# Kernel optimization log

Hardware: AMD Instinct MI355X
Metric: run time of the kernel (lower is better)

The kernel has to match this reference:

```python
import jax, jax.numpy as jnp
import numpy as np

N = 50000   # nodes
E = 640000  # edges
IN_C, HID_C, OUT_C = 128, 128, 64


def _glorot(key, shape):
    lim = float(np.sqrt(6.0 / (shape[0] + shape[1])))
    return jax.random.uniform(key, shape, jnp.float32, -lim, lim)


def setup_inputs() -> dict:
    key = jax.random.key(0)
    ks = jax.random.split(key, 6)
    x = jax.random.normal(ks[0], (N, IN_C), jnp.float32)
    edge_index = jax.random.randint(ks[1], (2, E), 0, N, dtype=jnp.int64)
    W1 = _glorot(ks[2], (IN_C, HID_C));  b1 = jnp.zeros((HID_C,), jnp.float32)
    W2 = _glorot(ks[3], (HID_C, HID_C)); b2 = jnp.zeros((HID_C,), jnp.float32)
    W3 = _glorot(ks[4], (HID_C, OUT_C)); b3 = jnp.zeros((OUT_C,), jnp.float32)
    return {"x": x, "edge_index": edge_index,
            "W1": W1, "b1": b1, "W2": W2, "b2": b2, "W3": W3, "b3": b3}


def gcn_conv(x, W, b, src, dst, n_nodes):
    """PyG GCNConv (eval): add self-loops, D^-1/2 (A+I) D^-1/2, linear, bias."""
    h = x @ W  # [N, out]
    ones = jnp.ones(src.shape[0], h.dtype)
    # degree including the self-loop (+1 per node)
    deg = jax.ops.segment_sum(ones, dst, num_segments=n_nodes) + 1.0
    dinv_sqrt = jax.lax.rsqrt(deg)
    coef = dinv_sqrt[src] * dinv_sqrt[dst]               # [E]
    agg = jax.ops.segment_sum(h[src] * coef[:, None], dst, num_segments=n_nodes)
    agg = agg + h * (1.0 / deg)[:, None]                 # self-loop term: 1/deg[i]
    return agg + b


def reference(x, edge_index, W1, b1, W2, b2, W3, b3):
    src, dst = edge_index[0], edge_index[1]
    h = jax.nn.relu(gcn_conv(x, W1, b1, src, dst, N))
    h = jax.nn.relu(gcn_conv(h, W2, b2, src, dst, N))
    return gcn_conv(h, W3, b3, src, dst, N)
```

## Files before the change

kernel.cpp:

```cpp
#include <hip/hip_runtime.h>


#define K_DIM 128

__device__ __forceinline__ unsigned short f2bf(float x) {
    unsigned u = __float_as_uint(x);
    return (unsigned short)((u + 0x7fffu + ((u >> 16) & 1u)) >> 16);
}
__device__ __forceinline__ float bflo(unsigned v) { return __uint_as_float(v << 16); }
__device__ __forceinline__ float bfhi(unsigned v) { return __uint_as_float(v & 0xffff0000u); }


__global__ void k_zero_int(int* __restrict__ p, int n) {
    int i = blockIdx.x * 256 + threadIdx.x;
    if (i < n) p[i] = 0;
}

__global__ void k_count(const int* __restrict__ dst, int* __restrict__ cnt, int E) {
    int e = blockIdx.x * 256 + threadIdx.x;
    if (e < E) atomicAdd(&cnt[dst[e]], 1);
}

__global__ void k_norms(const int* __restrict__ cnt, float* __restrict__ rsd, int n) {
    int i = blockIdx.x * 256 + threadIdx.x;
    if (i < n) rsd[i] = rsqrtf((float)cnt[i] + 1.0f);
}

__global__ void k_scan_block(const int* __restrict__ cnt, int* __restrict__ rowptr,
                             int* __restrict__ bsum, int n) {
    __shared__ int s[256];
    int t = threadIdx.x;
    int i = blockIdx.x * 256 + t;
    int x = (i < n) ? cnt[i] : 0;
    s[t] = x;
    __syncthreads();
#pragma unroll
    for (int d = 1; d < 256; d <<= 1) {
        int v = (t >= d) ? s[t - d] : 0;
        __syncthreads();
        s[t] += v;
        __syncthreads();
    }
    if (i < n) rowptr[i] = s[t] - x;
    if (t == 255) bsum[blockIdx.x] = s[255];
}

__global__ void k_scan_bsums(int* __restrict__ bsum, int nb) {
    __shared__ int s[256];
    int t = threadIdx.x;
    int x = (t < nb) ? bsum[t] : 0;
    s[t] = x;
    __syncthreads();
#pragma unroll
    for (int d = 1; d < 256; d <<= 1) {
        int v = (t >= d) ? s[t - d] : 0;
        __syncthreads();
        s[t] += v;
        __syncthreads();
    }
    if (t < nb) bsum[t] = s[t] - x;
}

__global__ void k_scan_add(int* __restrict__ rowptr, int* __restrict__ cursor,
                           const int* __restrict__ bsum, int n, int E) {
    int i = blockIdx.x * 256 + threadIdx.x;
    if (i < n) {
        int v = rowptr[i] + bsum[i >> 8];
        rowptr[i] = v;
        cursor[i] = v;
    }
    if (i == 0) rowptr[n] = E;
}

__global__ void k_fill(const int* __restrict__ src, const int* __restrict__ dst,
                       int* __restrict__ cursor, int* __restrict__ col, int E) {
    int e = blockIdx.x * 256 + threadIdx.x;
    if (e < E) {
        int d = dst[e];
        int pos = atomicAdd(&cursor[d], 1);
        col[pos] = src[e];
    }
}

template <int COUT>
__launch_bounds__(256)
__global__ void k_gemm1(const float* __restrict__ X, const float* __restrict__ W,
                        const float* __restrict__ rsd,
                        unsigned short* __restrict__ Hb, int nrows) {
    constexpr int BM = 64, BK = 32, TN = 4;
    constexpr int CG = COUT / TN;
    constexpr int RG = 256 / CG;
    constexpr int TM = BM / RG;
    constexpr int BMP = 68;

    __shared__ float Xs[BK][BMP];
    __shared__ float Ws[BK][COUT];

    const int tid = threadIdx.x;
    const int tx = tid % CG;
    const int ty = tid / CG;
    const int r0 = blockIdx.x * BM;

    float acc[TM][TN];
#pragma unroll
    for (int i = 0; i < TM; ++i)
#pragma unroll
        for (int j = 0; j < TN; ++j) acc[i][j] = 0.0f;

    for (int kb = 0; kb < K_DIM; kb += BK) {
        __syncthreads();
        {
            int r = tid >> 3, kq = tid & 7;
#pragma unroll
            for (int p = 0; p < 2; ++p) {
                int rr = r + p * 32;
                int grow = r0 + rr;
                if (grow >= nrows) grow = nrows - 1;
                float4 v = *(const float4*)&X[(size_t)grow * K_DIM + kb + kq * 4];
                Xs[kq * 4 + 0][rr] = v.x;
                Xs[kq * 4 + 1][rr] = v.y;
                Xs[kq * 4 + 2][rr] = v.z;
                Xs[kq * 4 + 3][rr] = v.w;
            }
        }
        {
            constexpr int F4 = COUT / 4;
            constexpr int RP = 256 / F4;
            int wq = tid % F4, wr = tid / F4;
#pragma unroll
            for (int p = 0; p < BK / RP; ++p) {
                int krow = wr + p * RP;
                *(float4*)&Ws[krow][wq * 4] =
                    *(const float4*)&W[(size_t)(kb + krow) * COUT + wq * 4];
            }
        }
        __syncthreads();
#pragma unroll
        for (int kk = 0; kk < BK; ++kk) {
            float4 w4 = *(const float4*)&Ws[kk][tx * TN];
            float a[TM];
#pragma unroll
            for (int i = 0; i < TM; i += 4) {
                float4 a4 = *(const float4*)&Xs[kk][ty * TM + i];
                a[i] = a4.x; a[i + 1] = a4.y; a[i + 2] = a4.z; a[i + 3] = a4.w;
            }
#pragma unroll
            for (int i = 0; i < TM; ++i) {
                acc[i][0] += a[i] * w4.x;
                acc[i][1] += a[i] * w4.y;
                acc[i][2] += a[i] * w4.z;
                acc[i][3] += a[i] * w4.w;
            }
        }
    }

#pragma unroll
    for (int i = 0; i < TM; ++i) {
        int row = r0 + ty * TM + i;
        if (row < nrows) {
            float rs = rsd[row];
            ushort4 hb;
            hb.x = f2bf(acc[i][0] * rs);
            hb.y = f2bf(acc[i][1] * rs);
            hb.z = f2bf(acc[i][2] * rs);
            hb.w = f2bf(acc[i][3] * rs);
            *(ushort4*)&Hb[(size_t)row * COUT + tx * TN] = hb;
        }
    }
}

template <int COUT>
__launch_bounds__(256)
__global__ void k_gemm_bf(const unsigned short* __restrict__ Ab, const float* __restrict__ W,
                          const float* __restrict__ rsd,
                          unsigned short* __restrict__ Hb, int nrows) {
    constexpr int BM = 64, BK = 32, TN = 4;
    constexpr int CG = COUT / TN;
    constexpr int RG = 256 / CG;
    constexpr int TM = BM / RG;
    constexpr int BMP = 68;

    __shared__ float Xs[BK][BMP];
    __shared__ float Ws[BK][COUT];

    const int tid = threadIdx.x;
    const int tx = tid % CG;
    const int ty = tid / CG;
    const int r0 = blockIdx.x * BM;

    float acc[TM][TN];
#pragma unroll
    for (int i = 0; i < TM; ++i)
#pragma unroll
        for (int j = 0; j < TN; ++j) acc[i][j] = 0.0f;

    for (int kb = 0; kb < K_DIM; kb += BK) {
        __syncthreads();
        {
            int r = tid >> 2, kq = tid & 3;
            int grow = r0 + r;
            if (grow >= nrows) grow = nrows - 1;
            uint4 v = *(const uint4*)&Ab[(size_t)grow * K_DIM + kb + kq * 8];
            int k0 = kq * 8;
            Xs[k0 + 0][r] = bflo(v.x); Xs[k0 + 1][r] = bfhi(v.x);
            Xs[k0 + 2][r] = bflo(v.y); Xs[k0 + 3][r] = bfhi(v.y);
            Xs[k0 + 4][r] = bflo(v.z); Xs[k0 + 5][r] = bfhi(v.z);
            Xs[k0 + 6][r] = bflo(v.w); Xs[k0 + 7][r] = bfhi(v.w);
        }
        {
            constexpr int F4 = COUT / 4;
            constexpr int RP = 256 / F4;
            int wq = tid % F4, wr = tid / F4;
#pragma unroll
            for (int p = 0; p < BK / RP; ++p) {
                int krow = wr + p * RP;
                *(float4*)&Ws[krow][wq * 4] =
                    *(const float4*)&W[(size_t)(kb + krow) * COUT + wq * 4];
            }
        }
        __syncthreads();
#pragma unroll
        for (int kk = 0; kk < BK; ++kk) {
            float4 w4 = *(const float4*)&Ws[kk][tx * TN];
            float a[TM];
#pragma unroll
            for (int i = 0; i < TM; i += 4) {
                float4 a4 = *(const float4*)&Xs[kk][ty * TM + i];
                a[i] = a4.x; a[i + 1] = a4.y; a[i + 2] = a4.z; a[i + 3] = a4.w;
            }
#pragma unroll
            for (int i = 0; i < TM; ++i) {
                acc[i][0] += a[i] * w4.x;
                acc[i][1] += a[i] * w4.y;
                acc[i][2] += a[i] * w4.z;
                acc[i][3] += a[i] * w4.w;
            }
        }
    }

#pragma unroll
    for (int i = 0; i < TM; ++i) {
        int row = r0 + ty * TM + i;
        if (row < nrows) {
            float rs = rsd[row];
            ushort4 hb;
            hb.x = f2bf(acc[i][0] * rs);
            hb.y = f2bf(acc[i][1] * rs);
            hb.z = f2bf(acc[i][2] * rs);
            hb.w = f2bf(acc[i][3] * rs);
            *(ushort4*)&Hb[(size_t)row * COUT + tx * TN] = hb;
        }
    }
}

template <int C>
__launch_bounds__(256)
__global__ void k_agg_bf(const unsigned short* __restrict__ Hb,
                         const int* __restrict__ rowptr, const int* __restrict__ col,
                         const float* __restrict__ rsd, const float* __restrict__ bias,
                         unsigned short* __restrict__ Ab, int n) {
    constexpr int TPN = C / 8;
    constexpr int NPB = 256 / TPN;
    const int node = blockIdx.x * NPB + threadIdx.x / TPN;
    const int c = (threadIdx.x % TPN) * 8;
    if (node >= n) return;

    float acc[8];
    {
        uint4 v = *(const uint4*)&Hb[(size_t)node * C + c];
        acc[0] = bflo(v.x); acc[1] = bfhi(v.x);
        acc[2] = bflo(v.y); acc[3] = bfhi(v.y);
        acc[4] = bflo(v.z); acc[5] = bfhi(v.z);
        acc[6] = bflo(v.w); acc[7] = bfhi(v.w);
    }
    int e = rowptr[node], end = rowptr[node + 1];
    for (; e + 1 < end; e += 2) {
        int s0 = col[e], s1 = col[e + 1];
        uint4 v0 = *(const uint4*)&Hb[(size_t)s0 * C + c];
        uint4 v1 = *(const uint4*)&Hb[(size_t)s1 * C + c];
        acc[0] += bflo(v0.x); acc[1] += bfhi(v0.x);
        acc[2] += bflo(v0.y); acc[3] += bfhi(v0.y);
        acc[4] += bflo(v0.z); acc[5] += bfhi(v0.z);
        acc[6] += bflo(v0.w); acc[7] += bfhi(v0.w);
        acc[0] += bflo(v1.x); acc[1] += bfhi(v1.x);
        acc[2] += bflo(v1.y); acc[3] += bfhi(v1.y);
        acc[4] += bflo(v1.z); acc[5] += bfhi(v1.z);
        acc[6] += bflo(v1.w); acc[7] += bfhi(v1.w);
    }
    if (e < end) {
        int s0 = col[e];
        uint4 v0 = *(const uint4*)&Hb[(size_t)s0 * C + c];
        acc[0] += bflo(v0.x); acc[1] += bfhi(v0.x);
        acc[2] += bflo(v0.y); acc[3] += bfhi(v0.y);
        acc[4] += bflo(v0.z); acc[5] += bfhi(v0.z);
        acc[6] += bflo(v0.w); acc[7] += bfhi(v0.w);
    }

    const float rs = rsd[node];
    const float4 b0 = *(const float4*)&bias[c];
    const float4 b1 = *(const float4*)&bias[c + 4];
    float r[8];
    r[0] = fmaxf(b0.x + rs * acc[0], 0.0f); r[1] = fmaxf(b0.y + rs * acc[1], 0.0f);
    r[2] = fmaxf(b0.z + rs * acc[2], 0.0f); r[3] = fmaxf(b0.w + rs * acc[3], 0.0f);
    r[4] = fmaxf(b1.x + rs * acc[4], 0.0f); r[5] = fmaxf(b1.y + rs * acc[5], 0.0f);
    r[6] = fmaxf(b1.z + rs * acc[6], 0.0f); r[7] = fmaxf(b1.w + rs * acc[7], 0.0f);

    uint4 o;
    o.x = (unsigned)f2bf(r[0]) | ((unsigned)f2bf(r[1]) << 16);
    o.y = (unsigned)f2bf(r[2]) | ((unsigned)f2bf(r[3]) << 16);
    o.z = (unsigned)f2bf(r[4]) | ((unsigned)f2bf(r[5]) << 16);
    o.w = (unsigned)f2bf(r[6]) | ((unsigned)f2bf(r[7]) << 16);
    *(uint4*)&Ab[(size_t)node * C + c] = o;
}

template <int C>
__launch_bounds__(256)
__global__ void k_agg_final(const unsigned short* __restrict__ Hb,
                            const int* __restrict__ rowptr, const int* __restrict__ col,
                            const float* __restrict__ rsd, const float* __restrict__ bias,
                            float* __restrict__ OUT, int n) {
    constexpr int TPN = C / 8;
    constexpr int NPB = 256 / TPN;
    const int node = blockIdx.x * NPB + threadIdx.x / TPN;
    const int c = (threadIdx.x % TPN) * 8;
    if (node >= n) return;

    float acc[8];
    {
        uint4 v = *(const uint4*)&Hb[(size_t)node * C + c];
        acc[0] = bflo(v.x); acc[1] = bfhi(v.x);
        acc[2] = bflo(v.y); acc[3] = bfhi(v.y);
        acc[4] = bflo(v.z); acc[5] = bfhi(v.z);
        acc[6] = bflo(v.w); acc[7] = bfhi(v.w);
    }
    int e = rowptr[node], end = rowptr[node + 1];
    for (; e + 1 < end; e += 2) {
        int s0 = col[e], s1 = col[e + 1];
        uint4 v0 = *(const uint4*)&Hb[(size_t)s0 * C + c];
        uint4 v1 = *(const uint4*)&Hb[(size_t)s1 * C + c];
        acc[0] += bflo(v0.x); acc[1] += bfhi(v0.x);
        acc[2] += bflo(v0.y); acc[3] += bfhi(v0.y);
        acc[4] += bflo(v0.z); acc[5] += bfhi(v0.z);
        acc[6] += bflo(v0.w); acc[7] += bfhi(v0.w);
        acc[0] += bflo(v1.x); acc[1] += bfhi(v1.x);
        acc[2] += bflo(v1.y); acc[3] += bfhi(v1.y);
        acc[4] += bflo(v1.z); acc[5] += bfhi(v1.z);
        acc[6] += bflo(v1.w); acc[7] += bfhi(v1.w);
    }
    if (e < end) {
        int s0 = col[e];
        uint4 v0 = *(const uint4*)&Hb[(size_t)s0 * C + c];
        acc[0] += bflo(v0.x); acc[1] += bfhi(v0.x);
        acc[2] += bflo(v0.y); acc[3] += bfhi(v0.y);
        acc[4] += bflo(v0.z); acc[5] += bfhi(v0.z);
        acc[6] += bflo(v0.w); acc[7] += bfhi(v0.w);
    }

    const float rs = rsd[node];
    const float4 b0 = *(const float4*)&bias[c];
    const float4 b1 = *(const float4*)&bias[c + 4];
    float* po = &OUT[(size_t)node * C + c];
    *(float4*)&po[0] = make_float4(b0.x + rs * acc[0], b0.y + rs * acc[1],
                                   b0.z + rs * acc[2], b0.w + rs * acc[3]);
    *(float4*)&po[4] = make_float4(b1.x + rs * acc[4], b1.y + rs * acc[5],
                                   b1.z + rs * acc[6], b1.w + rs * acc[7]);
}


extern "C" void kernel_launch(void* const* d_in, const int* in_sizes, int n_in,
                              void* d_out, int out_size, void* d_ws, size_t ws_size,
                              hipStream_t stream) {
    const float* x  = (const float*)d_in[0];
    const int*   ei = (const int*)d_in[1];
    const float* W1 = (const float*)d_in[2];
    const float* b1 = (const float*)d_in[3];
    const float* W2 = (const float*)d_in[4];
    const float* b2 = (const float*)d_in[5];
    const float* W3 = (const float*)d_in[6];
    const float* b3 = (const float*)d_in[7];

    const int N = in_sizes[0] / K_DIM;
    const int E = in_sizes[1] / 2;
    const int* srcv = ei;
    const int* dstv = ei + E;

    char* ws = (char*)d_ws;
    size_t off = 0;
    auto alloc = [&](size_t bytes) {
        char* p = ws + off;
        off += (bytes + 255) & ~(size_t)255;
        return p;
    };
    int*   cnt    = (int*)alloc((size_t)N * 4);
    int*   rowptr = (int*)alloc((size_t)(N + 1) * 4);
    int*   cursor = (int*)alloc((size_t)N * 4);
    int*   bsum   = (int*)alloc(256 * 4);
    float* rsd    = (float*)alloc((size_t)N * 4);
    int*   col    = (int*)alloc((size_t)E * 4);
    unsigned short* Hb1 = (unsigned short*)alloc((size_t)N * 128 * 2);
    unsigned short* Ab  = (unsigned short*)alloc((size_t)N * 128 * 2);
    unsigned short* Hb3 = (unsigned short*)alloc((size_t)N * 64 * 2);
    float* out = (float*)d_out;

    const int gN = (N + 255) / 256;
    const int gE = (E + 255) / 256;
    const int gb = (N + 63) / 64;
    const int nb = gN;
    const int gA128 = (N + 15) / 16;
    const int gAF   = (N + 31) / 32;

    k_zero_int<<<gN, 256, 0, stream>>>(cnt, N);
    k_count<<<gE, 256, 0, stream>>>(dstv, cnt, E);
    k_norms<<<gN, 256, 0, stream>>>(cnt, rsd, N);
    k_scan_block<<<nb, 256, 0, stream>>>(cnt, rowptr, bsum, N);
    k_scan_bsums<<<1, 256, 0, stream>>>(bsum, nb);
    k_scan_add<<<gN, 256, 0, stream>>>(rowptr, cursor, bsum, N, E);
    k_fill<<<gE, 256, 0, stream>>>(srcv, dstv, cursor, col, E);

    k_gemm1<128><<<gb, 256, 0, stream>>>(x, W1, rsd, Hb1, N);
    k_agg_bf<128><<<gA128, 256, 0, stream>>>(Hb1, rowptr, col, rsd, b1, Ab, N);

    k_gemm_bf<128><<<gb, 256, 0, stream>>>(Ab, W2, rsd, Hb1, N);
    k_agg_bf<128><<<gA128, 256, 0, stream>>>(Hb1, rowptr, col, rsd, b2, Ab, N);

    k_gemm_bf<64><<<gb, 256, 0, stream>>>(Ab, W3, rsd, Hb3, N);
    k_agg_final<64><<<gAF, 256, 0, stream>>>(Hb3, rowptr, col, rsd, b3, out, N);
}
```

Before: 299.9 us.

## Replace FP32 SIMT GEMMs with bf16 MFMA kernels and pre-converted weights

The three dense transforms now run on MFMA 16x16x32 bf16 matrix instructions in place of FP32 shared-memory tiled SIMT GEMMs. A new conversion kernel casts x to bf16 and transposes the weights into bf16 beforehand. The degree-norm computation is folded into the block scan kernel, which removes one launch. In exchange the first-layer input loses precision, one extra full pass over x is added, and the epilogue now issues scalar 2-byte stores.

```diff
diff --git a/kernel.cpp b/kernel.cpp
--- a/kernel.cpp
+++ b/kernel.cpp
@@ -2,6 +2,9 @@
 
 
 #define K_DIM 128
+
+typedef __attribute__((ext_vector_type(8))) short bf16x8;
+typedef __attribute__((ext_vector_type(4))) float f32x4;
 
 __device__ __forceinline__ unsigned short f2bf(float x) {
     unsigned u = __float_as_uint(x);
@@ -21,17 +24,13 @@
     if (e < E) atomicAdd(&cnt[dst[e]], 1);
 }
 
-__global__ void k_norms(const int* __restrict__ cnt, float* __restrict__ rsd, int n) {
-    int i = blockIdx.x * 256 + threadIdx.x;
-    if (i < n) rsd[i] = rsqrtf((float)cnt[i] + 1.0f);
-}
-
 __global__ void k_scan_block(const int* __restrict__ cnt, int* __restrict__ rowptr,
-                             int* __restrict__ bsum, int n) {
+                             int* __restrict__ bsum, float* __restrict__ rsd, int n) {
     __shared__ int s[256];
     int t = threadIdx.x;
     int i = blockIdx.x * 256 + t;
     int x = (i < n) ? cnt[i] : 0;
+    if (i < n) rsd[i] = rsqrtf((float)x + 1.0f);
     s[t] = x;
     __syncthreads();
 #pragma unroll
@@ -82,173 +81,75 @@
     }
 }
 
+__global__ void k_cvt(const float* __restrict__ x, unsigned short* __restrict__ Xb,
+                      const float* __restrict__ W1, const float* __restrict__ W2,
+                      const float* __restrict__ W3,
+                      unsigned short* __restrict__ Wt1, unsigned short* __restrict__ Wt2,
+                      unsigned short* __restrict__ Wt3, int nx4) {
+    int i = blockIdx.x * 256 + threadIdx.x;
+    if (i < nx4) {
+        float4 v = *(const float4*)&x[(size_t)i * 4];
+        ushort4 o;
+        o.x = f2bf(v.x); o.y = f2bf(v.y); o.z = f2bf(v.z); o.w = f2bf(v.w);
+        *(ushort4*)&Xb[(size_t)i * 4] = o;
+        return;
+    }
+    int j = i - nx4;
+    if (j < 16384) { int n = j >> 7, k = j & 127; Wt1[n * 128 + k] = f2bf(W1[k * 128 + n]); return; }
+    j -= 16384;
+    if (j < 16384) { int n = j >> 7, k = j & 127; Wt2[n * 128 + k] = f2bf(W2[k * 128 + n]); return; }
+    j -= 16384;
+    if (j < 8192)  { int n = j >> 7, k = j & 127; Wt3[n * 128 + k] = f2bf(W3[k * 64 + n]); return; }
+}
+
 template <int COUT>
 __launch_bounds__(256)
-__global__ void k_gemm1(const float* __restrict__ X, const float* __restrict__ W,
-                        const float* __restrict__ rsd,
-                        unsigned short* __restrict__ Hb, int nrows) {
-    constexpr int BM = 64, BK = 32, TN = 4;
-    constexpr int CG = COUT / TN;
-    constexpr int RG = 256 / CG;
-    constexpr int TM = BM / RG;
-    constexpr int BMP = 68;
-
-    __shared__ float Xs[BK][BMP];
-    __shared__ float Ws[BK][COUT];
-
-    const int tid = threadIdx.x;
-    const int tx = tid % CG;
-    const int ty = tid / CG;
-    const int r0 = blockIdx.x * BM;
-
-    float acc[TM][TN];
-#pragma unroll
-    for (int i = 0; i < TM; ++i)
-#pragma unroll
-        for (int j = 0; j < TN; ++j) acc[i][j] = 0.0f;
-
-    for (int kb = 0; kb < K_DIM; kb += BK) {
-        __syncthreads();
-        {
-            int r = tid >> 3, kq = tid & 7;
-#pragma unroll
-            for (int p = 0; p < 2; ++p) {
-                int rr = r + p * 32;
-                int grow = r0 + rr;
-                if (grow >= nrows) grow = nrows - 1;
-                float4 v = *(const float4*)&X[(size_t)grow * K_DIM + kb + kq * 4];
-                Xs[kq * 4 + 0][rr] = v.x;
-                Xs[kq * 4 + 1][rr] = v.y;
-                Xs[kq * 4 + 2][rr] = v.z;
-                Xs[kq * 4 + 3][rr] = v.w;
-            }
+__global__ void k_gemm_mfma(const unsigned short* __restrict__ A,
+                            const unsigned short* __restrict__ Wt,
+                            const float* __restrict__ rsd,
+                            unsigned short* __restrict__ Hb, int nrows) {
+    constexpr int NT = COUT / 16;
+    const int wave = threadIdx.x >> 6;
+    const int lane = threadIdx.x & 63;
+    const int m16 = lane & 15;
+    const int kg  = lane >> 4;
+    const int r0w = blockIdx.x * 64 + wave * 16;
+
+    int arow = r0w + m16;
+    if (arow >= nrows) arow = nrows - 1;
+
+    bf16x8 a[4];
+#pragma unroll
+    for (int kb = 0; kb < 4; ++kb)
+        a[kb] = *(const bf16x8*)&A[(size_t)arow * 128 + kb * 32 + kg * 8];
+
+    f32x4 acc[NT];
+#pragma unroll
+    for (int t = 0; t < NT; ++t) acc[t] = (f32x4){0.f, 0.f, 0.f, 0.f};
+
+#pragma unroll
+    for (int t = 0; t < NT; ++t) {
+        const unsigned short* wp = &Wt[(size_t)(t * 16 + m16) * 128 + kg * 8];
+#pragma unroll
+        for (int kb = 0; kb < 4; ++kb) {
+            bf16x8 b = *(const bf16x8*)&wp[kb * 32];
+            acc[t] = __builtin_amdgcn_mfma_f32_16x16x32_bf16(a[kb], b, acc[t], 0, 0, 0);
         }
-        {
-            constexpr int F4 = COUT / 4;
-            constexpr int RP = 256 / F4;
-            int wq = tid % F4, wr = tid / F4;
-#pragma unroll
-            for (int p = 0; p < BK / RP; ++p) {
-                int krow = wr + p * RP;
-                *(float4*)&Ws[krow][wq * 4] =
-                    *(const float4*)&W[(size_t)(kb + krow) * COUT + wq * 4];
-            }
-        }
-        __syncthreads();
-#pragma unroll
-        for (int kk = 0; kk < BK; ++kk) {
-            float4 w4 = *(const float4*)&Ws[kk][tx * TN];
-            float a[TM];
-#pragma unroll
-            for (int i = 0; i < TM; i += 4) {
-                float4 a4 = *(const float4*)&Xs[kk][ty * TM + i];
-                a[i] = a4.x; a[i + 1] = a4.y; a[i + 2] = a4.z; a[i + 3] = a4.w;
-            }
-#pragma unroll
-            for (int i = 0; i < TM; ++i) {
-                acc[i][0] += a[i] * w4.x;
-                acc[i][1] += a[i] * w4.y;
-                acc[i][2] += a[i] * w4.z;
-                acc[i][3] += a[i] * w4.w;
-            }
-        }
-    }
-
-#pragma unroll
-    for (int i = 0; i < TM; ++i) {
-        int row = r0 + ty * TM + i;
-        if (row < nrows) {
-            float rs = rsd[row];
-            ushort4 hb;
-            hb.x = f2bf(acc[i][0] * rs);
-            hb.y = f2bf(acc[i][1] * rs);
-            hb.z = f2bf(acc[i][2] * rs);
-            hb.w = f2bf(acc[i][3] * rs);
-            *(ushort4*)&Hb[(size_t)row * COUT + tx * TN] = hb;
-        }
-    }
-}
-
-template <int COUT>
-__launch_bounds__(256)
-__global__ void k_gemm_bf(const unsigned short* __restrict__ Ab, const float* __restrict__ W,
-                          const float* __restrict__ rsd,
-                          unsigned short* __restrict__ Hb, int nrows) {
-    constexpr int BM = 64, BK = 32, TN = 4;
-    constexpr int CG = COUT / TN;
-    constexpr int RG = 256 / CG;
-    constexpr int TM = BM / RG;
-    constexpr int BMP = 68;
-
-    __shared__ float Xs[BK][BMP];
-    __shared__ float Ws[BK][COUT];
-
-    const int tid = threadIdx.x;
-    const int tx = tid % CG;
-    const int ty = tid / CG;
-    const int r0 = blockIdx.x * BM;
-
-    float acc[TM][TN];
-#pragma unroll
-    for (int i = 0; i < TM; ++i)
-#pragma unroll
-        for (int j = 0; j < TN; ++j) acc[i][j] = 0.0f;
-
-    for (int kb = 0; kb < K_DIM; kb += BK) {
-        __syncthreads();
-        {
-            int r = tid >> 2, kq = tid & 3;
-            int grow = r0 + r;
-            if (grow >= nrows) grow = nrows - 1;
-            uint4 v = *(const uint4*)&Ab[(size_t)grow * K_DIM + kb + kq * 8];
-            int k0 = kq * 8;
-            Xs[k0 + 0][r] = bflo(v.x); Xs[k0 + 1][r] = bfhi(v.x);
-            Xs[k0 + 2][r] = bflo(v.y); Xs[k0 + 3][r] = bfhi(v.y);
-            Xs[k0 + 4][r] = bflo(v.z); Xs[k0 + 5][r] = bfhi(v.z);
-            Xs[k0 + 6][r] = bflo(v.w); Xs[k0 + 7][r] = bfhi(v.w);
-        }
-        {
-            constexpr int F4 = COUT / 4;
-            constexpr int RP = 256 / F4;
-            int wq = tid % F4, wr = tid / F4;
-#pragma unroll
-            for (int p = 0; p < BK / RP; ++p) {
-                int krow = wr + p * RP;
-                *(float4*)&Ws[krow][wq * 4] =
-                    *(const float4*)&W[(size_t)(kb + krow) * COUT + wq * 4];
-            }
-        }
-        __syncthreads();
-#pragma unroll
-        for (int kk = 0; kk < BK; ++kk) {
-            float4 w4 = *(const float4*)&Ws[kk][tx * TN];
-            float a[TM];
-#pragma unroll
-            for (int i = 0; i < TM; i += 4) {
-                float4 a4 = *(const float4*)&Xs[kk][ty * TM + i];
-                a[i] = a4.x; a[i + 1] = a4.y; a[i + 2] = a4.z; a[i + 3] = a4.w;
-            }
-#pragma unroll
-            for (int i = 0; i < TM; ++i) {
-                acc[i][0] += a[i] * w4.x;
-                acc[i][1] += a[i] * w4.y;
-                acc[i][2] += a[i] * w4.z;
-                acc[i][3] += a[i] * w4.w;
-            }
-        }
-    }
-
-#pragma unroll
-    for (int i = 0; i < TM; ++i) {
-        int row = r0 + ty * TM + i;
-        if (row < nrows) {
-            float rs = rsd[row];
-            ushort4 hb;
-            hb.x = f2bf(acc[i][0] * rs);
-            hb.y = f2bf(acc[i][1] * rs);
-            hb.z = f2bf(acc[i][2] * rs);
-            hb.w = f2bf(acc[i][3] * rs);
-            *(ushort4*)&Hb[(size_t)row * COUT + tx * TN] = hb;
+    }
+
+    const int rowb = r0w + kg * 4;
+    float rs[4];
+#pragma unroll
+    for (int i = 0; i < 4; ++i)
+        rs[i] = (rowb + i < nrows) ? rsd[rowb + i] : 0.0f;
+
+#pragma unroll
+    for (int t = 0; t < NT; ++t) {
+#pragma unroll
+        for (int i = 0; i < 4; ++i) {
+            int r = rowb + i;
+            if (r < nrows)
+                Hb[(size_t)r * COUT + t * 16 + m16] = f2bf(acc[t][i] * rs[i]);
         }
     }
 }
@@ -397,8 +298,13 @@
     int*   bsum   = (int*)alloc(256 * 4);
     float* rsd    = (float*)alloc((size_t)N * 4);
     int*   col    = (int*)alloc((size_t)E * 4);
+    unsigned short* Xb  = (unsigned short*)alloc((size_t)N * 128 * 2);
+    unsigned short* Wt1 = (unsigned short*)alloc(128 * 128 * 2);
+    unsigned short* Wt2 = (unsigned short*)alloc(128 * 128 * 2);
+    unsigned short* Wt3 = (unsigned short*)alloc(64 * 128 * 2);
     unsigned short* Hb1 = (unsigned short*)alloc((size_t)N * 128 * 2);
     unsigned short* Ab  = (unsigned short*)alloc((size_t)N * 128 * 2);
+    unsigned short* Hb2 = (unsigned short*)alloc((size_t)N * 128 * 2);
     unsigned short* Hb3 = (unsigned short*)alloc((size_t)N * 64 * 2);
     float* out = (float*)d_out;
 
@@ -408,21 +314,24 @@
     const int nb = gN;
     const int gA128 = (N + 15) / 16;
     const int gAF   = (N + 31) / 32;
+    const int nx4   = N * 32;
+    const int gCVT  = (nx4 + 16384 + 16384 + 8192 + 255) / 256;
 
     k_zero_int<<<gN, 256, 0, stream>>>(cnt, N);
     k_count<<<gE, 256, 0, stream>>>(dstv, cnt, E);
-    k_norms<<<gN, 256, 0, stream>>>(cnt, rsd, N);
-    k_scan_block<<<nb, 256, 0, stream>>>(cnt, rowptr, bsum, N);
+    k_scan_block<<<nb, 256, 0, stream>>>(cnt, rowptr, bsum, rsd, N);
     k_scan_bsums<<<1, 256, 0, stream>>>(bsum, nb);
     k_scan_add<<<gN, 256, 0, stream>>>(rowptr, cursor, bsum, N, E);
     k_fill<<<gE, 256, 0, stream>>>(srcv, dstv, cursor, col, E);
 
-    k_gemm1<128><<<gb, 256, 0, stream>>>(x, W1, rsd, Hb1, N);
+    k_cvt<<<gCVT, 256, 0, stream>>>(x, Xb, W1, W2, W3, Wt1, Wt2, Wt3, nx4);
+
+    k_gemm_mfma<128><<<gb, 256, 0, stream>>>(Xb, Wt1, rsd, Hb1, N);
     k_agg_bf<128><<<gA128, 256, 0, stream>>>(Hb1, rowptr, col, rsd, b1, Ab, N);
 
-    k_gemm_bf<128><<<gb, 256, 0, stream>>>(Ab, W2, rsd, Hb1, N);
-    k_agg_bf<128><<<gA128, 256, 0, stream>>>(Hb1, rowptr, col, rsd, b2, Ab, N);
-
-    k_gemm_bf<64><<<gb, 256, 0, stream>>>(Ab, W3, rsd, Hb3, N);
+    k_gemm_mfma<128><<<gb, 256, 0, stream>>>(Ab, Wt2, rsd, Hb2, N);
+    k_agg_bf<128><<<gA128, 256, 0, stream>>>(Hb2, rowptr, col, rsd, b2, Ab, N);
+
+    k_gemm_mfma<64><<<gb, 256, 0, stream>>>(Ab, Wt3, rsd, Hb3, N);
     k_agg_final<64><<<gAF, 256, 0, stream>>>(Hb3, rowptr, col, rsd, b3, out, N);
 }
```

New measurement: 288.5 us. -3.8%, faster.
